# Kernel optimization log

Measured on AMD Instinct MI355X. Metric: run time of the kernel, lower is better.

Reference implementation:

```python
import jax, jax.numpy as jnp
import numpy as np

TAU = 2.0
THR = 0.5
ALPHA = 4.0  # Sigmoid_Grad surrogate sharpness
EPS = 1e-5
HEADS = 16
SCALE = 0.25

@jax.custom_vjp
def spike(v):
    return (v > 0.0).astype(v.dtype)

def _spike_fwd(v):
    return (v > 0.0).astype(v.dtype), v

def _spike_bwd(v, g):
    s = jax.nn.sigmoid(ALPHA * v)
    return (g * ALPHA * s * (1.0 - s),)

spike.defvjp(_spike_fwd, _spike_bwd)

def lif(x):
    # x: (T, ...) ; stateful LIF over leading time dim, hard reset (detached spike)
    def step(mem, xt):
        mem = mem + (xt - mem) / TAU
        s = spike(mem - THR)
        mem = mem * (1.0 - jax.lax.stop_gradient(s))
        return mem, s
    _, s = jax.lax.scan(step, jnp.zeros_like(x[0]), x)
    return s

def bn(x, p):
    # x: (T,B,C,N), p: (4,C) = (gamma, beta, mean, var); inference-form BatchNorm1d
    g, b, m, v = p
    shp = (1, 1, -1, 1)
    return (x - m.reshape(shp)) * (g.reshape(shp) / jnp.sqrt(v.reshape(shp) + EPS)) + b.reshape(shp)

def conv_bn_lif(x, w, p, bias=None):
    # 1x1 Conv1d == channel matmul: (T,B,Cin,N) x (Cout,Cin) -> (T,B,Cout,N)
    y = jnp.einsum('tbcn,oc->tbon', x, w)
    if bias is not None:
        y = y + bias.reshape(1, 1, -1, 1)
    return lif(bn(y, p))

def _block(x, q_w, q_bn, k_w, k_bn, v_w, v_bn, proj_w, proj_bn,
           fc1_w, fc1_b, fc1_bn, fc2_w, fc2_b, fc2_bn):
    T, B, C, N = x.shape
    D = C // HEADS

    def to_heads(y):  # (T,B,C,N) -> (T,B,H,N,D)
        return y.transpose(0, 1, 3, 2).reshape(T, B, N, HEADS, D).transpose(0, 1, 3, 2, 4)

    q = to_heads(conv_bn_lif(x, q_w, q_bn))
    k = to_heads(conv_bn_lif(x, k_w, k_bn))
    v = to_heads(conv_bn_lif(x, v_w, v_bn))

    attn = jnp.einsum('tbhnd,tbhmd->tbhnm', q, k) * SCALE  # no softmax
    r = jnp.einsum('tbhnm,tbhmd->tbhnd', attn, v) * SCALE
    r = r.transpose(0, 1, 2, 4, 3).reshape(T, B, C, N)  # (T,B,H,D,N) -> (T,B,C,N)
    r = lif(r)  # attn_lif
    attn_out = conv_bn_lif(r, proj_w, proj_bn)  # proj conv+bn+lif

    x = x + attn_out  # residual 1

    h = conv_bn_lif(x, fc1_w, fc1_bn, fc1_b)
    m = conv_bn_lif(h, fc2_w, fc2_bn, fc2_b)
    return x + m  # residual 2

def setup_inputs() -> dict:
    key = jax.random.key(0)
    ks = jax.random.split(key, 16)
    T, B, C, N = 4, 16, 256, 512
    H = 1024  # mlp hidden = 4*C
    w = 0.05
    d = {}
    d['x'] = jax.random.normal(ks[0], (T, B, C, N), jnp.float32)
    d['q_w'] = jax.random.normal(ks[1], (C, C), jnp.float32) * w
    d['q_bn'] = jax.random.uniform(ks[2], (4, C), jnp.float32, 0.5, 1.5)
    d['k_w'] = jax.random.normal(ks[3], (C, C), jnp.float32) * w
    d['k_bn'] = jax.random.uniform(ks[4], (4, C), jnp.float32, 0.5, 1.5)
    d['v_w'] = jax.random.normal(ks[5], (C, C), jnp.float32) * w
    d['v_bn'] = jax.random.uniform(ks[6], (4, C), jnp.float32, 0.5, 1.5)
    d['proj_w'] = jax.random.normal(ks[7], (C, C), jnp.float32) * w
    d['proj_bn'] = jax.random.uniform(ks[8], (4, C), jnp.float32, 0.5, 1.5)
    d['fc1_w'] = jax.random.normal(ks[9], (H, C), jnp.float32) * w
    d['fc1_b'] = jnp.zeros((H,), jnp.float32)
    d['fc1_bn'] = jax.random.uniform(ks[10], (4, H), jnp.float32, 0.5, 1.5)
    d['fc2_w'] = jax.random.normal(ks[11], (C, H), jnp.float32) * w
    d['fc2_b'] = jnp.zeros((C,), jnp.float32)
    d['fc2_bn'] = jax.random.uniform(ks[12], (4, C), jnp.float32, 0.5, 1.5)
    return d

def reference(x, q_w, q_bn, k_w, k_bn, v_w, v_bn, proj_w, proj_bn,
              fc1_w, fc1_b, fc1_bn, fc2_w, fc2_b, fc2_bn):
    return _block(x, q_w, q_bn, k_w, k_bn, v_w, v_bn, proj_w, proj_bn,
                  fc1_w, fc1_b, fc1_bn, fc2_w, fc2_b, fc2_bn)
```

## Files before the change

### kernel.cpp

```cpp
#include <hip/hip_runtime.h>

#pragma clang fp contract(off)

typedef unsigned char u8;
typedef unsigned int u32;

#define TSTEPS 4

template <int P, int BK, int XMODE, bool HASX2, int OMODE, int NSEL>
__global__ __launch_bounds__(256) void conv_bn_lif(
    const void* __restrict__ X1v, const u8* __restrict__ X2,
    const float* __restrict__ W0, const float* __restrict__ W1,
    const float* __restrict__ W2, const float* __restrict__ bias,
    const float* __restrict__ bn0, const float* __restrict__ bn1,
    const float* __restrict__ bn2,
    u8* __restrict__ S0, u8* __restrict__ S1, u8* __restrict__ S2,
    const float* __restrict__ Xres, const u8* __restrict__ AOres,
    float* __restrict__ Fout,
    int Bsz, int Cin, int Cout, int N)
{
  constexpr int BO   = 16 * P;
  constexpr int BN   = 128;
  constexpr int TPR  = 256 / BK;
  constexpr int FPT  = BN / TPR;
  constexpr int NF4  = FPT / 4;
  static_assert(NF4 == 4, "loader assumes 16 elems/thread");
  constexpr int WPT  = BO * BK / 256;
  constexpr int NW4  = WPT / 4;
  constexpr int TPW  = BK / WPT;
  constexpr int WPAD = (P == 4) ? 4 : (P == 2) ? 2 : 0;
  constexpr int WROW = BO + WPAD;
  constexpr int XROWF = BN + 8;

  const int tid = threadIdx.x;
  const int tx = tid & 15, ty = tid >> 4;
  const int nBase = blockIdx.x * BN, b = blockIdx.z;

  int sel, oBase;
  if constexpr (NSEL == 3) {
    const int oT = gridDim.y / 3;
    sel = blockIdx.y / oT;
    oBase = (blockIdx.y - sel * oT) * BO;
  } else {
    sel = 0;
    oBase = blockIdx.y * BO;
  }
  const float* __restrict__ Wt  = (sel == 0) ? W0 : (sel == 1) ? W1 : W2;
  const float* __restrict__ bnp = (sel == 0) ? bn0 : (sel == 1) ? bn1 : bn2;
  u8* __restrict__ Sout         = (sel == 0) ? S0 : (sel == 1) ? S1 : S2;

  const int KT = Cin / BK;
  const int TT = TSTEPS * KT;

  __shared__ __align__(16) float Ws[2][BK][WROW];
  __shared__ __align__(16) u8 Xraw[(XMODE == 0) ? (2 * BK * XROWF * 4)
                                                : (2 * BK * BN)];
  __shared__ __align__(16) float BnL[BO][4];

  float* XF = (float*)Xraw;
  u8*    X8 = Xraw;

  if (tid < BO) {
    int o = oBase + tid;
    float g  = bnp[0 * Cout + o];
    float be = bnp[1 * Cout + o];
    float m  = bnp[2 * Cout + o];
    float vv = bnp[3 * Cout + o];
    float d_f = (float)((double)vv + (double)1e-5f);
    float s_f = (float)sqrt((double)d_f);
    BnL[tid][0] = (float)((double)g / (double)s_f);
    BnL[tid][1] = m;
    BnL[tid][2] = be;
    BnL[tid][3] = bias ? bias[o] : 0.0f;
  }

  float mem[P][8], acc[P][8];
  #pragma unroll
  for (int p = 0; p < P; ++p)
    #pragma unroll
    for (int q = 0; q < 8; ++q) { mem[p][q] = 0.0f; acc[p][q] = 0.0f; }

  const int xRow = tid / TPR;
  const int xcF  = (tid % TPR) * FPT;
  const int wO   = tid / TPW;
  const int wK   = (tid % TPW) * WPT;

  float4 px[NF4];
  u32    pxu[NF4];
  u32    pau[NF4];
  float4 pw[NW4];

  auto issue = [&](int i) {
    const int tI = i / KT, k0 = (i % KT) * BK;
    const size_t xb = (size_t)(tI * Bsz + b) * Cin * N
                    + (size_t)(k0 + xRow) * N + nBase + xcF;
    if constexpr (XMODE == 0) {
      const float* xp = (const float*)X1v + xb;
      #pragma unroll
      for (int f = 0; f < NF4; ++f) px[f] = *(const float4*)(xp + 4 * f);
    } else {
      uint4 u = *(const uint4*)((const u8*)X1v + xb);
      pxu[0] = u.x; pxu[1] = u.y; pxu[2] = u.z; pxu[3] = u.w;
    }
    if constexpr (HASX2) {
      uint4 u = *(const uint4*)(X2 + xb);
      pau[0] = u.x; pau[1] = u.y; pau[2] = u.z; pau[3] = u.w;
    }
    const size_t wb = (size_t)(oBase + wO) * Cin + k0 + wK;
    #pragma unroll
    for (int f = 0; f < NW4; ++f) pw[f] = *(const float4*)(Wt + wb + 4 * f);
  };

  auto commit = [&](int bf) {
    if constexpr (XMODE == 0) {
      #pragma unroll
      for (int f = 0; f < NF4; ++f) {
        float4 v = px[f];
        if constexpr (HASX2) {
          u32 a2 = pau[f];
          v.x = v.x + (float)(a2 & 0xffu);
          v.y = v.y + (float)((a2 >> 8) & 0xffu);
          v.z = v.z + (float)((a2 >> 16) & 0xffu);
          v.w = v.w + (float)((a2 >> 24) & 0xffu);
        }
        *(float4*)&XF[((size_t)(bf * BK + xRow)) * XROWF + xcF + 4 * f] = v;
      }
    } else {
      *(uint4*)&X8[(size_t)(bf * BK + xRow) * BN + xcF] =
          make_uint4(pxu[0], pxu[1], pxu[2], pxu[3]);
    }
    #pragma unroll
    for (int f = 0; f < NW4; ++f) {
      Ws[bf][wK + 4 * f + 0][wO] = pw[f].x;
      Ws[bf][wK + 4 * f + 1][wO] = pw[f].y;
      Ws[bf][wK + 4 * f + 2][wO] = pw[f].z;
      Ws[bf][wK + 4 * f + 3][wO] = pw[f].w;
    }
  };

  issue(0);
  commit(0);
  __syncthreads();

  for (int tt = 0; tt < TT; ++tt) {
    const int buf = tt & 1;
    if (tt + 1 < TT) issue(tt + 1);

    #pragma unroll
    for (int kk = 0; kk < BK; ++kk) {
      float xa[8];
      if constexpr (XMODE == 0) {
        float4 x0 = *(const float4*)&XF[(size_t)(buf * BK + kk) * XROWF + tx * 4];
        float4 x1 = *(const float4*)&XF[(size_t)(buf * BK + kk) * XROWF + 64 + tx * 4];
        xa[0] = x0.x; xa[1] = x0.y; xa[2] = x0.z; xa[3] = x0.w;
        xa[4] = x1.x; xa[5] = x1.y; xa[6] = x1.z; xa[7] = x1.w;
      } else {
        uint2 u = *(const uint2*)&X8[(size_t)(buf * BK + kk) * BN + tx * 8];
        #pragma unroll
        for (int j = 0; j < 4; ++j) xa[j]     = (float)((u.x >> (8 * j)) & 0xffu);
        #pragma unroll
        for (int j = 0; j < 4; ++j) xa[4 + j] = (float)((u.y >> (8 * j)) & 0xffu);
      }
      float wa[P];
      if constexpr (P == 2) {
        float2 w0 = *(const float2*)&Ws[buf][kk][ty * 2];
        wa[0] = w0.x; wa[1] = w0.y;
      } else {
        float4 w0 = *(const float4*)&Ws[buf][kk][ty * P];
        wa[0] = w0.x; wa[1] = w0.y; wa[2] = w0.z; wa[3] = w0.w;
        if constexpr (P == 8) {
          float4 w1 = *(const float4*)&Ws[buf][kk][ty * P + 4];
          wa[4] = w1.x; wa[5] = w1.y; wa[6] = w1.z; wa[7] = w1.w;
        }
      }
      #pragma unroll
      for (int p = 0; p < P; ++p)
        #pragma unroll
        for (int q = 0; q < 8; ++q)
          acc[p][q] = fmaf(wa[p], xa[q], acc[p][q]);
    }

    if ((tt % KT) == KT - 1) {
      const int t = tt / KT;
      const size_t sbase = (size_t)(t * Bsz + b) * Cout * N;
      #pragma unroll
      for (int p = 0; p < P; ++p) {
        const int o = oBase + ty * P + p;
        float4 bv = *(const float4*)&BnL[ty * P + p][0];
        bool spk[8];
        #pragma unroll
        for (int q = 0; q < 8; ++q) {
          float y = acc[p][q];
          if (bias) y = y + bv.w;
          float t1 = y - bv.y;
          float t2 = t1 * bv.x;
          y = t2 + bv.z;
          float m2 = mem[p][q];
          float dd = y - m2;
          m2 = m2 + dd * 0.5f;
          bool sp = (m2 - 0.5f) > 0.0f;
          mem[p][q] = sp ? 0.0f : m2;
          spk[q] = sp;
          acc[p][q] = 0.0f;
        }
        if constexpr (XMODE == 0) {
          const size_t rb0 = sbase + (size_t)o * N + nBase + tx * 4;
          u32 pk0 = 0, pk1 = 0;
          #pragma unroll
          for (int j = 0; j < 4; ++j) {
            if (spk[j])     pk0 |= (1u << (8 * j));
            if (spk[4 + j]) pk1 |= (1u << (8 * j));
          }
          *(u32*)&Sout[rb0]      = pk0;
          *(u32*)&Sout[rb0 + 64] = pk1;
        } else {
          const size_t rb = sbase + (size_t)o * N + nBase + tx * 8;
          if constexpr (OMODE == 0) {
            u32 pk0 = 0, pk1 = 0;
            #pragma unroll
            for (int j = 0; j < 4; ++j) {
              if (spk[j])     pk0 |= (1u << (8 * j));
              if (spk[4 + j]) pk1 |= (1u << (8 * j));
            }
            *(uint2*)&Sout[rb] = make_uint2(pk0, pk1);
          } else {
            float4 xr0 = *(const float4*)&Xres[rb];
            float4 xr1 = *(const float4*)&Xres[rb + 4];
            uint2 av = *(const uint2*)&AOres[rb];
            float xa4[8] = {xr0.x, xr0.y, xr0.z, xr0.w,
                            xr1.x, xr1.y, xr1.z, xr1.w};
            float o4[8];
            #pragma unroll
            for (int j = 0; j < 4; ++j) {
              float s = spk[j] ? 1.0f : 0.0f;
              float xn = xa4[j] + (float)((av.x >> (8 * j)) & 0xffu);
              o4[j] = xn + s;
            }
            #pragma unroll
            for (int j = 0; j < 4; ++j) {
              float s = spk[4 + j] ? 1.0f : 0.0f;
              float xn = xa4[4 + j] + (float)((av.y >> (8 * j)) & 0xffu);
              o4[4 + j] = xn + s;
            }
            *(float4*)&Fout[rb]     = make_float4(o4[0], o4[1], o4[2], o4[3]);
            *(float4*)&Fout[rb + 4] = make_float4(o4[4], o4[5], o4[6], o4[7]);
          }
        }
      }
    }

    __syncthreads();
    if (tt + 1 < TT) commit((tt + 1) & 1);
    __syncthreads();
  }
}

__global__ __launch_bounds__(256) void attn_lif(
    const u8* __restrict__ Qs, const u8* __restrict__ Ks,
    const u8* __restrict__ Vs, u8* __restrict__ Rs,
    int Bsz, int C, int N)
{
  const int tid = threadIdx.x;
  const int h = blockIdx.x & 15;
  const int b = blockIdx.x >> 4;

  __shared__ u8 qs[16][528];
  __shared__ u8 ks[16][528];
  __shared__ u8 vs[16][528];
  __shared__ int Gs[16][17];

  const int eG = tid >> 4;
  const int dG = tid & 15;
  const int dR = tid >> 4;
  const int nR0 = tid & 15;

  float mem[32];
  #pragma unroll
  for (int i = 0; i < 32; ++i) mem[i] = 0.0f;

  for (int t = 0; t < TSTEPS; ++t) {
    __syncthreads();
    const size_t base = ((size_t)(t * Bsz + b) * C + h * 16) * N;
    for (int i = 0; i < 32; ++i) {
      int flat = tid + 256 * i;
      int d = flat >> 9, n = flat & 511;
      size_t g = base + (size_t)d * N + n;
      qs[d][n] = Qs[g];
      ks[d][n] = Ks[g];
      vs[d][n] = Vs[g];
    }
    __syncthreads();

    int gi = 0;
    for (int n = 0; n < 512; ++n)
      gi += (int)ks[eG][n] * (int)vs[dG][n];
    Gs[eG][dG] = gi;
    __syncthreads();

    int Greg[16];
    #pragma unroll
    for (int e = 0; e < 16; ++e) Greg[e] = Gs[e][dR];

    const size_t obase = ((size_t)(t * Bsz + b) * C + h * 16 + dR) * N;
    for (int j = 0; j < 32; ++j) {
      int n = nR0 + 16 * j;
      int ri = 0;
      #pragma unroll
      for (int e = 0; e < 16; ++e)
        ri += qs[e][n] ? Greg[e] : 0;
      float r = (float)ri * 0.0625f;
      float m2 = mem[j];
      float d = r - m2;
      m2 = m2 + d * 0.5f;
      float s = (m2 - 0.5f) > 0.0f ? 1.0f : 0.0f;
      mem[j] = (s > 0.0f) ? 0.0f : m2;
      Rs[obase + n] = (s > 0.0f) ? (u8)1 : (u8)0;
    }
  }
}

extern "C" void kernel_launch(void* const* d_in, const int* in_sizes, int n_in,
                              void* d_out, int out_size, void* d_ws, size_t ws_size,
                              hipStream_t stream)
{
  const float* x     = (const float*)d_in[0];
  const float* q_w   = (const float*)d_in[1];
  const float* q_bn  = (const float*)d_in[2];
  const float* k_w   = (const float*)d_in[3];
  const float* k_bn  = (const float*)d_in[4];
  const float* v_w   = (const float*)d_in[5];
  const float* v_bn  = (const float*)d_in[6];
  const float* p_w   = (const float*)d_in[7];
  const float* p_bn  = (const float*)d_in[8];
  const float* f1_w  = (const float*)d_in[9];
  const float* f1_b  = (const float*)d_in[10];
  const float* f1_bn = (const float*)d_in[11];
  const float* f2_w  = (const float*)d_in[12];
  const float* f2_b  = (const float*)d_in[13];
  const float* f2_bn = (const float*)d_in[14];

  const int T = 4, B = 16, C = 256, N = 512, Hm = 1024;
  const size_t SZ = (size_t)T * B * C * N;

  char* ws = (char*)d_ws;
  u8* q_s  = (u8*)(ws + 0 * SZ);
  u8* k_s  = (u8*)(ws + 1 * SZ);
  u8* v_s  = (u8*)(ws + 2 * SZ);
  u8* r_s  = (u8*)(ws + 3 * SZ);
  u8* ao_s = (u8*)(ws + 4 * SZ);
  u8* h_s  = (u8*)(ws + 0 * SZ);

  dim3 blk(256);
  dim3 gQKV(N / 128, 3 * (C / 64), B);
  dim3 gP2(N / 128, C / 32, B);
  dim3 gF1(N / 128, Hm / 128, B);

  conv_bn_lif<4, 32, 0, false, 0, 3><<<gQKV, blk, 0, stream>>>(
      x, nullptr, q_w, k_w, v_w, nullptr, q_bn, k_bn, v_bn,
      q_s, k_s, v_s, nullptr, nullptr, nullptr, B, C, C, N);

  attn_lif<<<dim3(B * 16), blk, 0, stream>>>(q_s, k_s, v_s, r_s, B, C, N);

  conv_bn_lif<2, 32, 1, false, 0, 1><<<gP2, blk, 0, stream>>>(
      r_s, nullptr, p_w, p_w, p_w, nullptr, p_bn, p_bn, p_bn,
      ao_s, ao_s, ao_s, nullptr, nullptr, nullptr, B, C, C, N);
  conv_bn_lif<8, 32, 0, true, 0, 1><<<gF1, blk, 0, stream>>>(
      x, ao_s, f1_w, f1_w, f1_w, f1_b, f1_bn, f1_bn, f1_bn,
      h_s, h_s, h_s, nullptr, nullptr, nullptr, B, C, Hm, N);
  conv_bn_lif<2, 32, 1, false, 1, 1><<<gP2, blk, 0, stream>>>(
      h_s, nullptr, f2_w, f2_w, f2_w, f2_b, f2_bn, f2_bn, f2_bn,
      nullptr, nullptr, nullptr, x, ao_s, (float*)d_out, B, Hm, C, N);
}
```

Before: 985.1 us.

## Fuse Q/K/V projections per block to share X tile; drop redundant barrier

Each QKV block now computes all three projections (Q, K, V) for the same output-channel range. It keeps separate weight tiles, accumulators and membrane state per projection, so each float32 X tile is loaded and staged in shared memory once instead of three times. The redundant __syncthreads before the next-buffer commit is removed, which the double buffering makes safe. The byte-input projection and fc2 kernels move to a K-tile of 64 with multi-chunk loads. The cost is more registers and shared memory per block and fewer blocks in the QKV launch.

```diff
diff --git a/kernel.cpp b/kernel.cpp
--- a/kernel.cpp
+++ b/kernel.cpp
@@ -21,10 +21,10 @@
 {
   constexpr int BO   = 16 * P;
   constexpr int BN   = 128;
-  constexpr int TPR  = 256 / BK;
-  constexpr int FPT  = BN / TPR;
-  constexpr int NF4  = FPT / 4;
-  static_assert(NF4 == 4, "loader assumes 16 elems/thread");
+  constexpr int TPRX = 256 / BK;
+  constexpr int XPT  = BN / TPRX;
+  constexpr int NXC  = (XMODE == 0) ? XPT / 4 : XPT / 16;
+  static_assert(XMODE == 1 || (BK == 32 && NXC == 4), "f32 X needs BK=32");
   constexpr int WPT  = BO * BK / 256;
   constexpr int NW4  = WPT / 4;
   constexpr int TPW  = BK / WPT;
@@ -34,34 +34,26 @@
 
   const int tid = threadIdx.x;
   const int tx = tid & 15, ty = tid >> 4;
-  const int nBase = blockIdx.x * BN, b = blockIdx.z;
-
-  int sel, oBase;
-  if constexpr (NSEL == 3) {
-    const int oT = gridDim.y / 3;
-    sel = blockIdx.y / oT;
-    oBase = (blockIdx.y - sel * oT) * BO;
-  } else {
-    sel = 0;
-    oBase = blockIdx.y * BO;
-  }
-  const float* __restrict__ Wt  = (sel == 0) ? W0 : (sel == 1) ? W1 : W2;
-  const float* __restrict__ bnp = (sel == 0) ? bn0 : (sel == 1) ? bn1 : bn2;
-  u8* __restrict__ Sout         = (sel == 0) ? S0 : (sel == 1) ? S1 : S2;
+  const int nBase = blockIdx.x * BN, oBase = blockIdx.y * BO, b = blockIdx.z;
+
+  const float* Warr[3]  = {W0, W1, W2};
+  const float* bnArr[3] = {bn0, bn1, bn2};
+  u8*          Sarr[3]  = {S0, S1, S2};
 
   const int KT = Cin / BK;
   const int TT = TSTEPS * KT;
 
-  __shared__ __align__(16) float Ws[2][BK][WROW];
+  __shared__ __align__(16) float Ws[NSEL][2][BK][WROW];
   __shared__ __align__(16) u8 Xraw[(XMODE == 0) ? (2 * BK * XROWF * 4)
                                                 : (2 * BK * BN)];
-  __shared__ __align__(16) float BnL[BO][4];
+  __shared__ __align__(16) float BnL[NSEL * BO][4];
 
   float* XF = (float*)Xraw;
   u8*    X8 = Xraw;
 
-  if (tid < BO) {
-    int o = oBase + tid;
+  if (tid < NSEL * BO) {
+    const int s = tid / BO, oo = tid % BO, o = oBase + oo;
+    const float* bnp = bnArr[s];
     float g  = bnp[0 * Cout + o];
     float be = bnp[1 * Cout + o];
     float m  = bnp[2 * Cout + o];
@@ -74,47 +66,54 @@
     BnL[tid][3] = bias ? bias[o] : 0.0f;
   }
 
-  float mem[P][8], acc[P][8];
+  float mem[NSEL][P][8], acc[NSEL][P][8];
   #pragma unroll
-  for (int p = 0; p < P; ++p)
-    #pragma unroll
-    for (int q = 0; q < 8; ++q) { mem[p][q] = 0.0f; acc[p][q] = 0.0f; }
-
-  const int xRow = tid / TPR;
-  const int xcF  = (tid % TPR) * FPT;
+  for (int s = 0; s < NSEL; ++s)
+    #pragma unroll
+    for (int p = 0; p < P; ++p)
+      #pragma unroll
+      for (int q = 0; q < 8; ++q) { mem[s][p][q] = 0.0f; acc[s][p][q] = 0.0f; }
+
+  const int xRow = tid / TPRX;
+  const int xOff = (tid % TPRX) * XPT;
   const int wO   = tid / TPW;
   const int wK   = (tid % TPW) * WPT;
 
-  float4 px[NF4];
-  u32    pxu[NF4];
-  u32    pau[NF4];
-  float4 pw[NW4];
+  float4 px[NXC];
+  uint4  pxu[NXC];
+  u32    pau[4];
+  float4 pw[NSEL][NW4];
 
   auto issue = [&](int i) {
     const int tI = i / KT, k0 = (i % KT) * BK;
     const size_t xb = (size_t)(tI * Bsz + b) * Cin * N
-                    + (size_t)(k0 + xRow) * N + nBase + xcF;
+                    + (size_t)(k0 + xRow) * N + nBase + xOff;
     if constexpr (XMODE == 0) {
       const float* xp = (const float*)X1v + xb;
       #pragma unroll
-      for (int f = 0; f < NF4; ++f) px[f] = *(const float4*)(xp + 4 * f);
+      for (int f = 0; f < NXC; ++f) px[f] = *(const float4*)(xp + 4 * f);
     } else {
-      uint4 u = *(const uint4*)((const u8*)X1v + xb);
-      pxu[0] = u.x; pxu[1] = u.y; pxu[2] = u.z; pxu[3] = u.w;
+      const u8* xp = (const u8*)X1v + xb;
+      #pragma unroll
+      for (int f = 0; f < NXC; ++f) pxu[f] = *(const uint4*)(xp + 16 * f);
     }
     if constexpr (HASX2) {
       uint4 u = *(const uint4*)(X2 + xb);
       pau[0] = u.x; pau[1] = u.y; pau[2] = u.z; pau[3] = u.w;
     }
-    const size_t wb = (size_t)(oBase + wO) * Cin + k0 + wK;
-    #pragma unroll
-    for (int f = 0; f < NW4; ++f) pw[f] = *(const float4*)(Wt + wb + 4 * f);
+    #pragma unroll
+    for (int s = 0; s < NSEL; ++s) {
+      const size_t wb = (size_t)(oBase + wO) * Cin + k0 + wK;
+      #pragma unroll
+      for (int f = 0; f < NW4; ++f)
+        pw[s][f] = *(const float4*)(Warr[s] + wb + 4 * f);
+    }
   };
 
   auto commit = [&](int bf) {
     if constexpr (XMODE == 0) {
       #pragma unroll
-      for (int f = 0; f < NF4; ++f) {
+      for (int f = 0; f < NXC; ++f) {
         float4 v = px[f];
         if constexpr (HASX2) {
           u32 a2 = pau[f];
@@ -123,19 +122,22 @@
           v.z = v.z + (float)((a2 >> 16) & 0xffu);
           v.w = v.w + (float)((a2 >> 24) & 0xffu);
         }
-        *(float4*)&XF[((size_t)(bf * BK + xRow)) * XROWF + xcF + 4 * f] = v;
+        *(float4*)&XF[((size_t)(bf * BK + xRow)) * XROWF + xOff + 4 * f] = v;
       }
     } else {
-      *(uint4*)&X8[(size_t)(bf * BK + xRow) * BN + xcF] =
-          make_uint4(pxu[0], pxu[1], pxu[2], pxu[3]);
-    }
-    #pragma unroll
-    for (int f = 0; f < NW4; ++f) {
-      Ws[bf][wK + 4 * f + 0][wO] = pw[f].x;
-      Ws[bf][wK + 4 * f + 1][wO] = pw[f].y;
-      Ws[bf][wK + 4 * f + 2][wO] = pw[f].z;
-      Ws[bf][wK + 4 * f + 3][wO] = pw[f].w;
-    }
+      #pragma unroll
+      for (int f = 0; f < NXC; ++f)
+        *(uint4*)&X8[(size_t)(bf * BK + xRow) * BN + xOff + 16 * f] = pxu[f];
+    }
+    #pragma unroll
+    for (int s = 0; s < NSEL; ++s)
+      #pragma unroll
+      for (int f = 0; f < NW4; ++f) {
+        Ws[s][bf][wK + 4 * f + 0][wO] = pw[s][f].x;
+        Ws[s][bf][wK + 4 * f + 1][wO] = pw[s][f].y;
+        Ws[s][bf][wK + 4 * f + 2][wO] = pw[s][f].z;
+        Ws[s][bf][wK + 4 * f + 3][wO] = pw[s][f].w;
+      }
   };
 
   issue(0);
@@ -161,95 +163,103 @@
         #pragma unroll
         for (int j = 0; j < 4; ++j) xa[4 + j] = (float)((u.y >> (8 * j)) & 0xffu);
       }
-      float wa[P];
-      if constexpr (P == 2) {
-        float2 w0 = *(const float2*)&Ws[buf][kk][ty * 2];
-        wa[0] = w0.x; wa[1] = w0.y;
-      } else {
-        float4 w0 = *(const float4*)&Ws[buf][kk][ty * P];
-        wa[0] = w0.x; wa[1] = w0.y; wa[2] = w0.z; wa[3] = w0.w;
-        if constexpr (P == 8) {
-          float4 w1 = *(const float4*)&Ws[buf][kk][ty * P + 4];
-          wa[4] = w1.x; wa[5] = w1.y; wa[6] = w1.z; wa[7] = w1.w;
+      float wa[NSEL][P];
+      #pragma unroll
+      for (int s = 0; s < NSEL; ++s) {
+        if constexpr (P == 2) {
+          float2 w0 = *(const float2*)&Ws[s][buf][kk][ty * 2];
+          wa[s][0] = w0.x; wa[s][1] = w0.y;
+        } else {
+          float4 w0 = *(const float4*)&Ws[s][buf][kk][ty * P];
+          wa[s][0] = w0.x; wa[s][1] = w0.y; wa[s][2] = w0.z; wa[s][3] = w0.w;
+          if constexpr (P == 8) {
+            float4 w1 = *(const float4*)&Ws[s][buf][kk][ty * P + 4];
+            wa[s][4] = w1.x; wa[s][5] = w1.y; wa[s][6] = w1.z; wa[s][7] = w1.w;
+          }
         }
       }
       #pragma unroll
-      for (int p = 0; p < P; ++p)
+      for (int s = 0; s < NSEL; ++s)
         #pragma unroll
-        for (int q = 0; q < 8; ++q)
-          acc[p][q] = fmaf(wa[p], xa[q], acc[p][q]);
+        for (int p = 0; p < P; ++p)
+          #pragma unroll
+          for (int q = 0; q < 8; ++q)
+            acc[s][p][q] = fmaf(wa[s][p], xa[q], acc[s][p][q]);
     }
 
     if ((tt % KT) == KT - 1) {
       const int t = tt / KT;
       const size_t sbase = (size_t)(t * Bsz + b) * Cout * N;
       #pragma unroll
-      for (int p = 0; p < P; ++p) {
-        const int o = oBase + ty * P + p;
-        float4 bv = *(const float4*)&BnL[ty * P + p][0];
-        bool spk[8];
+      for (int s = 0; s < NSEL; ++s) {
+        u8* __restrict__ Sout = Sarr[s];
         #pragma unroll
-        for (int q = 0; q < 8; ++q) {
-          float y = acc[p][q];
-          if (bias) y = y + bv.w;
-          float t1 = y - bv.y;
-          float t2 = t1 * bv.x;
-          y = t2 + bv.z;
-          float m2 = mem[p][q];
-          float dd = y - m2;
-          m2 = m2 + dd * 0.5f;
-          bool sp = (m2 - 0.5f) > 0.0f;
-          mem[p][q] = sp ? 0.0f : m2;
-          spk[q] = sp;
-          acc[p][q] = 0.0f;
-        }
-        if constexpr (XMODE == 0) {
-          const size_t rb0 = sbase + (size_t)o * N + nBase + tx * 4;
-          u32 pk0 = 0, pk1 = 0;
+        for (int p = 0; p < P; ++p) {
+          const int o = oBase + ty * P + p;
+          float4 bv = *(const float4*)&BnL[s * BO + ty * P + p][0];
+          bool spk[8];
           #pragma unroll
-          for (int j = 0; j < 4; ++j) {
-            if (spk[j])     pk0 |= (1u << (8 * j));
-            if (spk[4 + j]) pk1 |= (1u << (8 * j));
+          for (int q = 0; q < 8; ++q) {
+            float y = acc[s][p][q];
+            if (bias) y = y + bv.w;
+            float t1 = y - bv.y;
+            float t2 = t1 * bv.x;
+            y = t2 + bv.z;
+            float m2 = mem[s][p][q];
+            float dd = y - m2;
+            m2 = m2 + dd * 0.5f;
+            bool sp = (m2 - 0.5f) > 0.0f;
+            mem[s][p][q] = sp ? 0.0f : m2;
+            spk[q] = sp;
+            acc[s][p][q] = 0.0f;
           }
-          *(u32*)&Sout[rb0]      = pk0;
-          *(u32*)&Sout[rb0 + 64] = pk1;
-        } else {
-          const size_t rb = sbase + (size_t)o * N + nBase + tx * 8;
-          if constexpr (OMODE == 0) {
+          if constexpr (XMODE == 0) {
+            const size_t rb0 = sbase + (size_t)o * N + nBase + tx * 4;
             u32 pk0 = 0, pk1 = 0;
             #pragma unroll
             for (int j = 0; j < 4; ++j) {
               if (spk[j])     pk0 |= (1u << (8 * j));
               if (spk[4 + j]) pk1 |= (1u << (8 * j));
             }
-            *(uint2*)&Sout[rb] = make_uint2(pk0, pk1);
+            *(u32*)&Sout[rb0]      = pk0;
+            *(u32*)&Sout[rb0 + 64] = pk1;
           } else {
-            float4 xr0 = *(const float4*)&Xres[rb];
-            float4 xr1 = *(const float4*)&Xres[rb + 4];
-            uint2 av = *(const uint2*)&AOres[rb];
-            float xa4[8] = {xr0.x, xr0.y, xr0.z, xr0.w,
-                            xr1.x, xr1.y, xr1.z, xr1.w};
-            float o4[8];
-            #pragma unroll
-            for (int j = 0; j < 4; ++j) {
-              float s = spk[j] ? 1.0f : 0.0f;
-              float xn = xa4[j] + (float)((av.x >> (8 * j)) & 0xffu);
-              o4[j] = xn + s;
+            const size_t rb = sbase + (size_t)o * N + nBase + tx * 8;
+            if constexpr (OMODE == 0) {
+              u32 pk0 = 0, pk1 = 0;
+              #pragma unroll
+              for (int j = 0; j < 4; ++j) {
+                if (spk[j])     pk0 |= (1u << (8 * j));
+                if (spk[4 + j]) pk1 |= (1u << (8 * j));
+              }
+              *(uint2*)&Sout[rb] = make_uint2(pk0, pk1);
+            } else {
+              float4 xr0 = *(const float4*)&Xres[rb];
+              float4 xr1 = *(const float4*)&Xres[rb + 4];
+              uint2 av = *(const uint2*)&AOres[rb];
+              float xa4[8] = {xr0.x, xr0.y, xr0.z, xr0.w,
+                              xr1.x, xr1.y, xr1.z, xr1.w};
+              float o4[8];
+              #pragma unroll
+              for (int j = 0; j < 4; ++j) {
+                float sv = spk[j] ? 1.0f : 0.0f;
+                float xn = xa4[j] + (float)((av.x >> (8 * j)) & 0xffu);
+                o4[j] = xn + sv;
+              }
+              #pragma unroll
+              for (int j = 0; j < 4; ++j) {
+                float sv = spk[4 + j] ? 1.0f : 0.0f;
+                float xn = xa4[4 + j] + (float)((av.y >> (8 * j)) & 0xffu);
+                o4[4 + j] = xn + sv;
+              }
+              *(float4*)&Fout[rb]     = make_float4(o4[0], o4[1], o4[2], o4[3]);
+              *(float4*)&Fout[rb + 4] = make_float4(o4[4], o4[5], o4[6], o4[7]);
             }
-            #pragma unroll
-            for (int j = 0; j < 4; ++j) {
-              float s = spk[4 + j] ? 1.0f : 0.0f;
-              float xn = xa4[4 + j] + (float)((av.y >> (8 * j)) & 0xffu);
-              o4[4 + j] = xn + s;
-            }
-            *(float4*)&Fout[rb]     = make_float4(o4[0], o4[1], o4[2], o4[3]);
-            *(float4*)&Fout[rb + 4] = make_float4(o4[4], o4[5], o4[6], o4[7]);
           }
         }
       }
     }
 
-    __syncthreads();
     if (tt + 1 < TT) commit((tt + 1) & 1);
     __syncthreads();
   }
@@ -351,23 +361,23 @@
   u8* h_s  = (u8*)(ws + 0 * SZ);
 
   dim3 blk(256);
-  dim3 gQKV(N / 128, 3 * (C / 64), B);
+  dim3 gQKV(N / 128, C / 32, B);
   dim3 gP2(N / 128, C / 32, B);
   dim3 gF1(N / 128, Hm / 128, B);
 
-  conv_bn_lif<4, 32, 0, false, 0, 3><<<gQKV, blk, 0, stream>>>(
+  conv_bn_lif<2, 32, 0, false, 0, 3><<<gQKV, blk, 0, stream>>>(
       x, nullptr, q_w, k_w, v_w, nullptr, q_bn, k_bn, v_bn,
       q_s, k_s, v_s, nullptr, nullptr, nullptr, B, C, C, N);
 
   attn_lif<<<dim3(B * 16), blk, 0, stream>>>(q_s, k_s, v_s, r_s, B, C, N);
 
-  conv_bn_lif<2, 32, 1, false, 0, 1><<<gP2, blk, 0, stream>>>(
+  conv_bn_lif<2, 64, 1, false, 0, 1><<<gP2, blk, 0, stream>>>(
       r_s, nullptr, p_w, p_w, p_w, nullptr, p_bn, p_bn, p_bn,
       ao_s, ao_s, ao_s, nullptr, nullptr, nullptr, B, C, C, N);
   conv_bn_lif<8, 32, 0, true, 0, 1><<<gF1, blk, 0, stream>>>(
       x, ao_s, f1_w, f1_w, f1_w, f1_b, f1_bn, f1_bn, f1_bn,
       h_s, h_s, h_s, nullptr, nullptr, nullptr, B, C, Hm, N);
-  conv_bn_lif<2, 32, 1, false, 1, 1><<<gP2, blk, 0, stream>>>(
+  conv_bn_lif<2, 64, 1, false, 1, 1><<<gP2, blk, 0, stream>>>(
       h_s, nullptr, f2_w, f2_w, f2_w, f2_b, f2_bn, f2_bn, f2_bn,
       nullptr, nullptr, nullptr, x, ao_s, (float*)d_out, B, Hm, C, N);
 }
```

Measured after the change: 1.069 ms. 1.08x slower.

## Split conv+LIF into time-parallel conv kernels and separate LIF scan kernels

Applied to the files above, without the earlier changes.

Adds a new path, used when the workspace is large enough, that runs each 1x1 conv+BN as a GEMM spread across T*B blocks writing float pre-activations. Separate elementwise lif_scan kernels then apply the LIF recurrence over the four timesteps. This gives each conv four times as many blocks and removes the serial time loop inside them, at the cost of writing and rereading large float intermediates in global memory plus extra launches. The fallback path also switches two byte-input convs to BK=64 and drops one barrier in the fused kernel.

```diff
diff --git a/kernel.cpp b/kernel.cpp
--- a/kernel.cpp
+++ b/kernel.cpp
@@ -21,10 +21,10 @@
 {
   constexpr int BO   = 16 * P;
   constexpr int BN   = 128;
-  constexpr int TPR  = 256 / BK;
-  constexpr int FPT  = BN / TPR;
-  constexpr int NF4  = FPT / 4;
-  static_assert(NF4 == 4, "loader assumes 16 elems/thread");
+  constexpr int TPRX = 256 / BK;
+  constexpr int XPT  = BN / TPRX;
+  constexpr int NXC  = (XMODE == 0) ? XPT / 4 : XPT / 16;
+  static_assert(XMODE == 1 || (BK == 32 && NXC == 4), "f32 X needs BK=32");
   constexpr int WPT  = BO * BK / 256;
   constexpr int NW4  = WPT / 4;
   constexpr int TPW  = BK / WPT;
@@ -80,27 +80,28 @@
     #pragma unroll
     for (int q = 0; q < 8; ++q) { mem[p][q] = 0.0f; acc[p][q] = 0.0f; }
 
-  const int xRow = tid / TPR;
-  const int xcF  = (tid % TPR) * FPT;
+  const int xRow = tid / TPRX;
+  const int xOff = (tid % TPRX) * XPT;
   const int wO   = tid / TPW;
   const int wK   = (tid % TPW) * WPT;
 
-  float4 px[NF4];
-  u32    pxu[NF4];
-  u32    pau[NF4];
+  float4 px[(XMODE == 0) ? NXC : 1];
+  uint4  pxu[(XMODE == 1) ? NXC : 1];
+  u32    pau[4];
   float4 pw[NW4];
 
   auto issue = [&](int i) {
     const int tI = i / KT, k0 = (i % KT) * BK;
     const size_t xb = (size_t)(tI * Bsz + b) * Cin * N
-                    + (size_t)(k0 + xRow) * N + nBase + xcF;
+                    + (size_t)(k0 + xRow) * N + nBase + xOff;
     if constexpr (XMODE == 0) {
       const float* xp = (const float*)X1v + xb;
       #pragma unroll
-      for (int f = 0; f < NF4; ++f) px[f] = *(const float4*)(xp + 4 * f);
+      for (int f = 0; f < NXC; ++f) px[f] = *(const float4*)(xp + 4 * f);
     } else {
-      uint4 u = *(const uint4*)((const u8*)X1v + xb);
-      pxu[0] = u.x; pxu[1] = u.y; pxu[2] = u.z; pxu[3] = u.w;
+      const u8* xp = (const u8*)X1v + xb;
+      #pragma unroll
+      for (int f = 0; f < NXC; ++f) pxu[f] = *(const uint4*)(xp + 16 * f);
     }
     if constexpr (HASX2) {
       uint4 u = *(const uint4*)(X2 + xb);
@@ -114,7 +115,7 @@
   auto commit = [&](int bf) {
     if constexpr (XMODE == 0) {
       #pragma unroll
-      for (int f = 0; f < NF4; ++f) {
+      for (int f = 0; f < NXC; ++f) {
         float4 v = px[f];
         if constexpr (HASX2) {
           u32 a2 = pau[f];
@@ -123,11 +124,12 @@
           v.z = v.z + (float)((a2 >> 16) & 0xffu);
           v.w = v.w + (float)((a2 >> 24) & 0xffu);
         }
-        *(float4*)&XF[((size_t)(bf * BK + xRow)) * XROWF + xcF + 4 * f] = v;
+        *(float4*)&XF[((size_t)(bf * BK + xRow)) * XROWF + xOff + 4 * f] = v;
       }
     } else {
-      *(uint4*)&X8[(size_t)(bf * BK + xRow) * BN + xcF] =
-          make_uint4(pxu[0], pxu[1], pxu[2], pxu[3]);
+      #pragma unroll
+      for (int f = 0; f < NXC; ++f)
+        *(uint4*)&X8[(size_t)(bf * BK + xRow) * BN + xOff + 16 * f] = pxu[f];
     }
     #pragma unroll
     for (int f = 0; f < NW4; ++f) {
@@ -232,15 +234,15 @@
             float o4[8];
             #pragma unroll
             for (int j = 0; j < 4; ++j) {
-              float s = spk[j] ? 1.0f : 0.0f;
+              float sv = spk[j] ? 1.0f : 0.0f;
               float xn = xa4[j] + (float)((av.x >> (8 * j)) & 0xffu);
-              o4[j] = xn + s;
+              o4[j] = xn + sv;
             }
             #pragma unroll
             for (int j = 0; j < 4; ++j) {
-              float s = spk[4 + j] ? 1.0f : 0.0f;
+              float sv = spk[4 + j] ? 1.0f : 0.0f;
               float xn = xa4[4 + j] + (float)((av.y >> (8 * j)) & 0xffu);
-              o4[4 + j] = xn + s;
+              o4[4 + j] = xn + sv;
             }
             *(float4*)&Fout[rb]     = make_float4(o4[0], o4[1], o4[2], o4[3]);
             *(float4*)&Fout[rb + 4] = make_float4(o4[4], o4[5], o4[6], o4[7]);
@@ -249,9 +251,272 @@
       }
     }
 
-    __syncthreads();
     if (tt + 1 < TT) commit((tt + 1) & 1);
     __syncthreads();
+  }
+}
+
+template <int P, int BK, int XMODE, bool HASX2, int NSEL>
+__global__ __launch_bounds__(256) void conv_bn_t(
+    const void* __restrict__ X1v, const u8* __restrict__ X2,
+    const float* __restrict__ W0, const float* __restrict__ W1,
+    const float* __restrict__ W2, const float* __restrict__ bias,
+    const float* __restrict__ bn0, const float* __restrict__ bn1,
+    const float* __restrict__ bn2,
+    float* __restrict__ Y0, float* __restrict__ Y1, float* __restrict__ Y2,
+    int Bsz, int Cin, int Cout, int N)
+{
+  constexpr int BO   = 16 * P;
+  constexpr int BN   = 128;
+  constexpr int TPRX = 256 / BK;
+  constexpr int XPT  = BN / TPRX;
+  constexpr int NXC  = (XMODE == 0) ? XPT / 4 : XPT / 16;
+  static_assert(XMODE == 1 || (BK == 32 && NXC == 4), "f32 X needs BK=32");
+  constexpr int WPT  = BO * BK / 256;
+  constexpr int NW4  = WPT / 4;
+  constexpr int TPW  = BK / WPT;
+  constexpr int WPAD = (P == 4) ? 4 : (P == 2) ? 2 : 0;
+  constexpr int WROW = BO + WPAD;
+  constexpr int XROWF = BN + 8;
+
+  const int tid = threadIdx.x;
+  const int tx = tid & 15, ty = tid >> 4;
+  const int nBase = blockIdx.x * BN;
+  const int zb = blockIdx.z;
+  const int tI = zb / Bsz, b = zb % Bsz;
+
+  int sel, oBase;
+  if constexpr (NSEL == 3) {
+    const int oT = gridDim.y / 3;
+    sel = blockIdx.y / oT;
+    oBase = (blockIdx.y - sel * oT) * BO;
+  } else {
+    sel = 0;
+    oBase = blockIdx.y * BO;
+  }
+  const float* __restrict__ Wt  = (sel == 0) ? W0 : (sel == 1) ? W1 : W2;
+  const float* __restrict__ bnp = (sel == 0) ? bn0 : (sel == 1) ? bn1 : bn2;
+  float* __restrict__ Yout      = (sel == 0) ? Y0 : (sel == 1) ? Y1 : Y2;
+
+  const int KT = Cin / BK;
+
+  __shared__ __align__(16) float Ws[2][BK][WROW];
+  __shared__ __align__(16) u8 Xraw[(XMODE == 0) ? (2 * BK * XROWF * 4)
+                                                : (2 * BK * BN)];
+  __shared__ __align__(16) float BnL[BO][4];
+
+  float* XF = (float*)Xraw;
+  u8*    X8 = Xraw;
+
+  if (tid < BO) {
+    int o = oBase + tid;
+    float g  = bnp[0 * Cout + o];
+    float be = bnp[1 * Cout + o];
+    float m  = bnp[2 * Cout + o];
+    float vv = bnp[3 * Cout + o];
+    float d_f = (float)((double)vv + (double)1e-5f);
+    float s_f = (float)sqrt((double)d_f);
+    BnL[tid][0] = (float)((double)g / (double)s_f);
+    BnL[tid][1] = m;
+    BnL[tid][2] = be;
+    BnL[tid][3] = bias ? bias[o] : 0.0f;
+  }
+
+  float acc[P][8];
+  #pragma unroll
+  for (int p = 0; p < P; ++p)
+    #pragma unroll
+    for (int q = 0; q < 8; ++q) acc[p][q] = 0.0f;
+
+  const int xRow = tid / TPRX;
+  const int xOff = (tid % TPRX) * XPT;
+  const int wO   = tid / TPW;
+  const int wK   = (tid % TPW) * WPT;
+
+  float4 px[(XMODE == 0) ? NXC : 1];
+  uint4  pxu[(XMODE == 1) ? NXC : 1];
+  u32    pau[4];
+  float4 pw[NW4];
+
+  auto issue = [&](int i) {
+    const int k0 = i * BK;
+    const size_t xb = (size_t)(tI * Bsz + b) * Cin * N
+                    + (size_t)(k0 + xRow) * N + nBase + xOff;
+    if constexpr (XMODE == 0) {
+      const float* xp = (const float*)X1v + xb;
+      #pragma unroll
+      for (int f = 0; f < NXC; ++f) px[f] = *(const float4*)(xp + 4 * f);
+    } else {
+      const u8* xp = (const u8*)X1v + xb;
+      #pragma unroll
+      for (int f = 0; f < NXC; ++f) pxu[f] = *(const uint4*)(xp + 16 * f);
+    }
+    if constexpr (HASX2) {
+      uint4 u = *(const uint4*)(X2 + xb);
+      pau[0] = u.x; pau[1] = u.y; pau[2] = u.z; pau[3] = u.w;
+    }
+    const size_t wb = (size_t)(oBase + wO) * Cin + k0 + wK;
+    #pragma unroll
+    for (int f = 0; f < NW4; ++f) pw[f] = *(const float4*)(Wt + wb + 4 * f);
+  };
+
+  auto commit = [&](int bf) {
+    if constexpr (XMODE == 0) {
+      #pragma unroll
+      for (int f = 0; f < NXC; ++f) {
+        float4 v = px[f];
+        if constexpr (HASX2) {
+          u32 a2 = pau[f];
+          v.x = v.x + (float)(a2 & 0xffu);
+          v.y = v.y + (float)((a2 >> 8) & 0xffu);
+          v.z = v.z + (float)((a2 >> 16) & 0xffu);
+          v.w = v.w + (float)((a2 >> 24) & 0xffu);
+        }
+        *(float4*)&XF[((size_t)(bf * BK + xRow)) * XROWF + xOff + 4 * f] = v;
+      }
+    } else {
+      #pragma unroll
+      for (int f = 0; f < NXC; ++f)
+        *(uint4*)&X8[(size_t)(bf * BK + xRow) * BN + xOff + 16 * f] = pxu[f];
+    }
+    #pragma unroll
+    for (int f = 0; f < NW4; ++f) {
+      Ws[bf][wK + 4 * f + 0][wO] = pw[f].x;
+      Ws[bf][wK + 4 * f + 1][wO] = pw[f].y;
+      Ws[bf][wK + 4 * f + 2][wO] = pw[f].z;
+      Ws[bf][wK + 4 * f + 3][wO] = pw[f].w;
+    }
+  };
+
+  issue(0);
+  commit(0);
+  __syncthreads();
+
+  for (int tt = 0; tt < KT; ++tt) {
+    const int buf = tt & 1;
+    if (tt + 1 < KT) issue(tt + 1);
+
+    #pragma unroll
+    for (int kk = 0; kk < BK; ++kk) {
+      float xa[8];
+      if constexpr (XMODE == 0) {
+        float4 x0 = *(const float4*)&XF[(size_t)(buf * BK + kk) * XROWF + tx * 4];
+        float4 x1 = *(const float4*)&XF[(size_t)(buf * BK + kk) * XROWF + 64 + tx * 4];
+        xa[0] = x0.x; xa[1] = x0.y; xa[2] = x0.z; xa[3] = x0.w;
+        xa[4] = x1.x; xa[5] = x1.y; xa[6] = x1.z; xa[7] = x1.w;
+      } else {
+        uint2 u = *(const uint2*)&X8[(size_t)(buf * BK + kk) * BN + tx * 8];
+        #pragma unroll
+        for (int j = 0; j < 4; ++j) xa[j]     = (float)((u.x >> (8 * j)) & 0xffu);
+        #pragma unroll
+        for (int j = 0; j < 4; ++j) xa[4 + j] = (float)((u.y >> (8 * j)) & 0xffu);
+      }
+      float wa[P];
+      if constexpr (P == 2) {
+        float2 w0 = *(const float2*)&Ws[buf][kk][ty * 2];
+        wa[0] = w0.x; wa[1] = w0.y;
+      } else {
+        float4 w0 = *(const float4*)&Ws[buf][kk][ty * P];
+        wa[0] = w0.x; wa[1] = w0.y; wa[2] = w0.z; wa[3] = w0.w;
+        if constexpr (P == 8) {
+          float4 w1 = *(const float4*)&Ws[buf][kk][ty * P + 4];
+          wa[4] = w1.x; wa[5] = w1.y; wa[6] = w1.z; wa[7] = w1.w;
+        }
+      }
+      #pragma unroll
+      for (int p = 0; p < P; ++p)
+        #pragma unroll
+        for (int q = 0; q < 8; ++q)
+          acc[p][q] = fmaf(wa[p], xa[q], acc[p][q]);
+    }
+
+    if (tt + 1 < KT) {
+      commit((tt + 1) & 1);
+      __syncthreads();
+    }
+  }
+
+  const size_t sbase = (size_t)(tI * Bsz + b) * Cout * N;
+  #pragma unroll
+  for (int p = 0; p < P; ++p) {
+    const int o = oBase + ty * P + p;
+    float4 bv = *(const float4*)&BnL[ty * P + p][0];
+    float o4[8];
+    #pragma unroll
+    for (int q = 0; q < 8; ++q) {
+      float y = acc[p][q];
+      if (bias) y = y + bv.w;
+      float t1 = y - bv.y;
+      float t2 = t1 * bv.x;
+      o4[q] = t2 + bv.z;
+    }
+    if constexpr (XMODE == 0) {
+      const size_t rb0 = sbase + (size_t)o * N + nBase + tx * 4;
+      *(float4*)&Yout[rb0]      = make_float4(o4[0], o4[1], o4[2], o4[3]);
+      *(float4*)&Yout[rb0 + 64] = make_float4(o4[4], o4[5], o4[6], o4[7]);
+    } else {
+      const size_t rb = sbase + (size_t)o * N + nBase + tx * 8;
+      *(float4*)&Yout[rb]     = make_float4(o4[0], o4[1], o4[2], o4[3]);
+      *(float4*)&Yout[rb + 4] = make_float4(o4[4], o4[5], o4[6], o4[7]);
+    }
+  }
+}
+
+template <int NSEL, int FMODE>
+__global__ __launch_bounds__(256) void lif_scan(
+    const float* __restrict__ Y0, const float* __restrict__ Y1,
+    const float* __restrict__ Y2,
+    u8* __restrict__ S0, u8* __restrict__ S1, u8* __restrict__ S2,
+    const float* __restrict__ Xres, const u8* __restrict__ AOres,
+    float* __restrict__ Fout, int Bsz, int cnShift)
+{
+  const size_t off = ((size_t)blockIdx.x * 256 + threadIdx.x) * 4;
+  const size_t stride = (size_t)Bsz << cnShift;
+  const float* Ya[3] = {Y0, Y1, Y2};
+  u8* Sa[3] = {S0, S1, S2};
+
+  float mem[NSEL][4];
+  #pragma unroll
+  for (int s = 0; s < NSEL; ++s)
+    #pragma unroll
+    for (int j = 0; j < 4; ++j) mem[s][j] = 0.0f;
+
+  for (int t = 0; t < TSTEPS; ++t) {
+    const size_t pos = off + (size_t)t * stride;
+    #pragma unroll
+    for (int s = 0; s < NSEL; ++s) {
+      float4 yv = *(const float4*)(Ya[s] + pos);
+      float ya[4] = {yv.x, yv.y, yv.z, yv.w};
+      bool spk[4];
+      #pragma unroll
+      for (int j = 0; j < 4; ++j) {
+        float m2 = mem[s][j];
+        float dd = ya[j] - m2;
+        m2 = m2 + dd * 0.5f;
+        bool sp = (m2 - 0.5f) > 0.0f;
+        mem[s][j] = sp ? 0.0f : m2;
+        spk[j] = sp;
+      }
+      if constexpr (FMODE == 0) {
+        u32 pack = 0;
+        #pragma unroll
+        for (int j = 0; j < 4; ++j)
+          if (spk[j]) pack |= (1u << (8 * j));
+        *(u32*)&Sa[s][pos] = pack;
+      } else {
+        float4 xr = *(const float4*)(Xres + pos);
+        u32 av = *(const u32*)(AOres + pos);
+        float xa4[4] = {xr.x, xr.y, xr.z, xr.w};
+        float o4[4];
+        #pragma unroll
+        for (int j = 0; j < 4; ++j) {
+          float sv = spk[j] ? 1.0f : 0.0f;
+          float xn = xa4[j] + (float)((av >> (8 * j)) & 0xffu);
+          o4[j] = xn + sv;
+        }
+        *(float4*)&Fout[pos] = make_float4(o4[0], o4[1], o4[2], o4[3]);
+      }
+    }
   }
 }
 
@@ -351,23 +616,73 @@
   u8* h_s  = (u8*)(ws + 0 * SZ);
 
   dim3 blk(256);
-  dim3 gQKV(N / 128, 3 * (C / 64), B);
-  dim3 gP2(N / 128, C / 32, B);
-  dim3 gF1(N / 128, Hm / 128, B);
-
-  conv_bn_lif<4, 32, 0, false, 0, 3><<<gQKV, blk, 0, stream>>>(
-      x, nullptr, q_w, k_w, v_w, nullptr, q_bn, k_bn, v_bn,
-      q_s, k_s, v_s, nullptr, nullptr, nullptr, B, C, C, N);
-
-  attn_lif<<<dim3(B * 16), blk, 0, stream>>>(q_s, k_s, v_s, r_s, B, C, N);
-
-  conv_bn_lif<2, 32, 1, false, 0, 1><<<gP2, blk, 0, stream>>>(
-      r_s, nullptr, p_w, p_w, p_w, nullptr, p_bn, p_bn, p_bn,
-      ao_s, ao_s, ao_s, nullptr, nullptr, nullptr, B, C, C, N);
-  conv_bn_lif<8, 32, 0, true, 0, 1><<<gF1, blk, 0, stream>>>(
-      x, ao_s, f1_w, f1_w, f1_w, f1_b, f1_bn, f1_bn, f1_bn,
-      h_s, h_s, h_s, nullptr, nullptr, nullptr, B, C, Hm, N);
-  conv_bn_lif<2, 32, 1, false, 1, 1><<<gP2, blk, 0, stream>>>(
-      h_s, nullptr, f2_w, f2_w, f2_w, f2_b, f2_bn, f2_bn, f2_bn,
-      nullptr, nullptr, nullptr, x, ao_s, (float*)d_out, B, Hm, C, N);
+
+  const size_t NEED = 21 * SZ;
+
+  if (ws_size >= NEED) {
+    float* yA = (float*)(ws + 5 * SZ);
+    float* yq = yA;
+    float* yk = yA + SZ;
+    float* yv = yA + 2 * SZ;
+    float* yp = yA;
+    float* yh = yA;
+    float* yo = yA;
+
+    dim3 gQKV(N / 128, 3 * (C / 64), T * B);
+    dim3 gP(N / 128, C / 32, T * B);
+    dim3 gF1(N / 128, Hm / 128, T * B);
+    const int sC = 17;
+    const int sH = 19;
+    dim3 gScanC((B << sC) / 1024);
+    dim3 gScanH((B << sH) / 1024);
+
+    conv_bn_t<4, 32, 0, false, 3><<<gQKV, blk, 0, stream>>>(
+        x, nullptr, q_w, k_w, v_w, nullptr, q_bn, k_bn, v_bn,
+        yq, yk, yv, B, C, C, N);
+    lif_scan<3, 0><<<gScanC, blk, 0, stream>>>(
+        yq, yk, yv, q_s, k_s, v_s, nullptr, nullptr, nullptr, B, sC);
+
+    attn_lif<<<dim3(B * 16), blk, 0, stream>>>(q_s, k_s, v_s, r_s, B, C, N);
+
+    conv_bn_t<2, 32, 1, false, 1><<<gP, blk, 0, stream>>>(
+        r_s, nullptr, p_w, p_w, p_w, nullptr, p_bn, p_bn, p_bn,
+        yp, yp, yp, B, C, C, N);
+    lif_scan<1, 0><<<gScanC, blk, 0, stream>>>(
+        yp, nullptr, nullptr, ao_s, nullptr, nullptr, nullptr, nullptr,
+        nullptr, B, sC);
+
+    conv_bn_t<8, 32, 0, true, 1><<<gF1, blk, 0, stream>>>(
+        x, ao_s, f1_w, f1_w, f1_w, f1_b, f1_bn, f1_bn, f1_bn,
+        yh, yh, yh, B, C, Hm, N);
+    lif_scan<1, 0><<<gScanH, blk, 0, stream>>>(
+        yh, nullptr, nullptr, h_s, nullptr, nullptr, nullptr, nullptr,
+        nullptr, B, sH);
+
+    conv_bn_t<2, 32, 1, false, 1><<<gP, blk, 0, stream>>>(
+        h_s, nullptr, f2_w, f2_w, f2_w, f2_b, f2_bn, f2_bn, f2_bn,
+        yo, yo, yo, B, Hm, C, N);
+    lif_scan<1, 1><<<gScanC, blk, 0, stream>>>(
+        yo, nullptr, nullptr, nullptr, nullptr, nullptr, x, ao_s,
+        (float*)d_out, B, sC);
+  } else {
+    dim3 gQKV(N / 128, 3 * (C / 64), B);
+    dim3 gP2(N / 128, C / 32, B);
+    dim3 gF1(N / 128, Hm / 128, B);
+
+    conv_bn_lif<4, 32, 0, false, 0, 3><<<gQKV, blk, 0, stream>>>(
+        x, nullptr, q_w, k_w, v_w, nullptr, q_bn, k_bn, v_bn,
+        q_s, k_s, v_s, nullptr, nullptr, nullptr, B, C, C, N);
+
+    attn_lif<<<dim3(B * 16), blk, 0, stream>>>(q_s, k_s, v_s, r_s, B, C, N);
+
+    conv_bn_lif<2, 64, 1, false, 0, 1><<<gP2, blk, 0, stream>>>(
+        r_s, nullptr, p_w, p_w, p_w, nullptr, p_bn, p_bn, p_bn,
+        ao_s, ao_s, ao_s, nullptr, nullptr, nullptr, B, C, C, N);
+    conv_bn_lif<8, 32, 0, true, 0, 1><<<gF1, blk, 0, stream>>>(
+        x, ao_s, f1_w, f1_w, f1_w, f1_b, f1_bn, f1_bn, f1_bn,
+        h_s, h_s, h_s, nullptr, nullptr, nullptr, B, C, Hm, N);
+    conv_bn_lif<2, 64, 1, false, 1, 1><<<gP2, blk, 0, stream>>>(
+        h_s, nullptr, f2_w, f2_w, f2_w, f2_b, f2_bn, f2_bn, f2_bn,
+        nullptr, nullptr, nullptr, x, ao_s, (float*)d_out, B, Hm, C, N);
+  }
 }
```

After: 1.730 ms. 75.6% more time.
